# Optimization experiments

Measured on AMD Instinct MI355X. Metric: run time of the kernel, lower is better.

The kernel has to match this reference:

```python
import jax, jax.numpy as jnp
import numpy as np

N = 500_000          # total nodes (25000 graphs x 20 joints)
E = 800_000          # total edges (25000 graphs x 32 edges)
NUM_EDGES = 32       # edges per graph (module init arg)
IN_C = 128
OUT_C = 256
LN_EPS = 1e-5


def setup_inputs() -> dict:
    key = jax.random.key(0)
    ks = jax.random.split(key, 8)
    x = jax.random.normal(ks[0], (N, IN_C), dtype=jnp.float32)
    edge_index = jax.random.randint(ks[1], (2, E), 0, N, dtype=jnp.int64)
    # learned per-graph edge weights (init ones in torch; randomized positive here)
    edge_weights = jax.random.uniform(ks[2], (NUM_EDGES,), jnp.float32, 0.5, 1.5)
    W_gcn = jax.random.normal(ks[3], (IN_C, OUT_C), jnp.float32) / np.float32(np.sqrt(IN_C))
    b_gcn = jnp.zeros((OUT_C,), jnp.float32)
    W_res = jax.random.normal(ks[4], (IN_C, OUT_C), jnp.float32) / np.float32(np.sqrt(IN_C))
    b_res = jnp.zeros((OUT_C,), jnp.float32)
    gamma = jnp.ones((OUT_C,), jnp.float32)
    beta = jnp.zeros((OUT_C,), jnp.float32)
    return dict(x=x, edge_weights=edge_weights, W_gcn=W_gcn, b_gcn=b_gcn,
                W_res=W_res, b_res=b_res, gamma=gamma, beta=beta,
                edge_index=edge_index)


def reference(x, edge_weights, W_gcn, b_gcn, W_res, b_res, gamma, beta, edge_index):
    n = x.shape[0]
    e_tot = edge_index.shape[1]
    batch_size = e_tot // NUM_EDGES
    ew = jnp.tile(edge_weights, batch_size)            # repeated per-batch weights [E]
    row, col = edge_index[0], edge_index[1]            # source -> target

    # GCN symmetric normalization with implicit self loops (weight 1)
    deg = jax.ops.segment_sum(ew, col, num_segments=n) + 1.0   # [N]
    dinv = jax.lax.rsqrt(deg)                                   # [N]
    norm = dinv[row] * ew * dinv[col]                           # [E]

    xw = x @ W_gcn                                              # [N, OUT_C]
    agg = jax.ops.segment_sum(norm[:, None] * xw[row], col, num_segments=n)
    # self-loop contribution: norm_ii = dinv_i * 1 * dinv_i = 1/deg_i
    gcn_out = agg + xw * (dinv * dinv)[:, None] + b_gcn         # [N, OUT_C]

    res = x @ W_res + b_res                                     # residual Linear
    h = gcn_out + res

    mu = jnp.mean(h, axis=-1, keepdims=True)
    var = jnp.mean((h - mu) ** 2, axis=-1, keepdims=True)
    hn = (h - mu) * jax.lax.rsqrt(var + LN_EPS)
    return jax.nn.relu(hn * gamma + beta)
```

## Files before the change

kernel.cpp:

```cpp
#include <hip/hip_runtime.h>
#include <hip/hip_bf16.h>

typedef __attribute__((ext_vector_type(8))) short short8;
typedef __attribute__((ext_vector_type(4))) float f32x4;
typedef unsigned short u16;

#define IN_C 128
#define OUT_C 256
#define LN_EPS 1e-5f
#define CHUNK 320

__device__ __forceinline__ u16 f2bf(float f) {
    __hip_bfloat16 h = __float2bfloat16(f);
    return __builtin_bit_cast(u16, h);
}

__global__ void k_count(const int* __restrict__ ei, const float* __restrict__ ew,
                        float* __restrict__ deg, int* __restrict__ cnt, int E) {
    int e = blockIdx.x * 256 + threadIdx.x;
    if (e < E) {
        int c = ei[E + e];
        atomicAdd(&deg[c], ew[e & 31]);
        atomicAdd(&cnt[c], 1);
    }
}

__global__ void k_dinv(float* __restrict__ deg, int n) {
    int i = blockIdx.x * 256 + threadIdx.x;
    if (i < n) deg[i] = rsqrtf(1.0f + deg[i]);
}

__global__ void k_scan1(const int* __restrict__ cnt, int* __restrict__ partial, int n) {
    __shared__ int sm[256];
    int b = blockIdx.x, t = threadIdx.x;
    int base = b * 1024 + t * 4;
    int s = 0;
#pragma unroll
    for (int k = 0; k < 4; ++k) { int i = base + k; if (i < n) s += cnt[i]; }
    sm[t] = s; __syncthreads();
    for (int m = 128; m > 0; m >>= 1) { if (t < m) sm[t] += sm[t + m]; __syncthreads(); }
    if (t == 0) partial[b] = sm[0];
}

__global__ void k_scan2(int* __restrict__ partial, int nb) {
    __shared__ int sm[512];
    int t = threadIdx.x;
    sm[t] = (t < nb) ? partial[t] : 0;
    __syncthreads();
    for (int d = 1; d < 512; d <<= 1) {
        int v = (t >= d) ? sm[t - d] : 0;
        __syncthreads();
        sm[t] += v;
        __syncthreads();
    }
    if (t < nb) partial[t] = (t == 0) ? 0 : sm[t - 1];
}

__global__ void k_scan3(const int* __restrict__ cnt, const int* __restrict__ partial,
                        int* __restrict__ off, int* __restrict__ cur, int n, int E) {
    __shared__ int sm[256];
    int b = blockIdx.x, t = threadIdx.x;
    int base = b * 1024 + t * 4;
    int c[4]; int s = 0;
#pragma unroll
    for (int k = 0; k < 4; ++k) { int i = base + k; c[k] = (i < n) ? cnt[i] : 0; s += c[k]; }
    sm[t] = s; __syncthreads();
    for (int d = 1; d < 256; d <<= 1) {
        int v = (t >= d) ? sm[t - d] : 0;
        __syncthreads();
        sm[t] += v;
        __syncthreads();
    }
    int run = partial[b] + (sm[t] - s);
#pragma unroll
    for (int k = 0; k < 4; ++k) {
        int i = base + k;
        if (i < n) { off[i] = run; cur[i] = run; }
        run += c[k];
    }
    if (b == 0 && t == 0) off[n] = E;
}

__global__ void k_place(const int* __restrict__ ei, const float* __restrict__ ew,
                        const float* __restrict__ dinv, int* __restrict__ cur,
                        int4* __restrict__ rec4, int E) {
    int e = blockIdx.x * 256 + threadIdx.x;
    if (e >= E) return;
    int r = ei[e], c = ei[E + e];
    float nrm = dinv[r] * ew[e & 31] * dinv[c];
    int p = atomicAdd(&cur[c], 1);
    rec4[p] = make_int4(r, c, __float_as_int(nrm), 0);
}

__global__ void k_wprep(const float* __restrict__ Wg, const float* __restrict__ Wr,
                        const float* __restrict__ bg, const float* __restrict__ br,
                        u16* __restrict__ wfrag, float* __restrict__ bc) {
    int tid = blockIdx.x * 256 + threadIdx.x;
    if (tid < OUT_C) bc[tid] = bg[tid] + br[tid];
    if (tid >= 8192) return;
    int l = tid & 63;
    int t = (tid >> 6) & 15;
    int s = tid >> 10;
    int n = t * 16 + (l & 15);
    int k0 = s * 32 + (l >> 4) * 8;
    short8 pk;
#pragma unroll
    for (int j = 0; j < 8; ++j) {
        int k = k0 + j;
        float w = (k < IN_C) ? Wg[k * OUT_C + n] : Wr[(k - IN_C) * OUT_C + n];
        pk[j] = (short)f2bf(w);
    }
    reinterpret_cast<short8*>(wfrag)[tid] = pk;
}

__global__ __launch_bounds__(512, 4) void k_gemm(
    const float4* __restrict__ x4, const float* __restrict__ dinv,
    const int* __restrict__ off, const int4* __restrict__ rec4,
    const u16* __restrict__ wfrag, const float* __restrict__ bc,
    const float* __restrict__ gamma, const float* __restrict__ beta,
    float* __restrict__ out, int N) {

    __shared__ u16 A[32 * 264];
    __shared__ float red[8 * 32 * 2];
    __shared__ float fin[32 * 2];
    __shared__ int4 recs[CHUNK];

    const int tid = threadIdx.x;
    const int lane = tid & 63;
    const int wv = tid >> 6;
    const long r0 = (long)blockIdx.x * 32;

    const int trow = tid >> 4;
    const int tq = tid & 15;
    const long gr = r0 + trow;

    float ua[8];
    int p0 = 0, p1 = 0;
    {
        u16* xp = &A[trow * 264 + 128 + tq * 8];
        if (gr < N) {
            float d = dinv[gr];
            float d2 = d * d;
            const float4* xs = x4 + gr * 32 + tq * 2;
            float4 v0 = xs[0], v1 = xs[1];
            ushort4 x0, x1;
            x0.x = f2bf(v0.x); x0.y = f2bf(v0.y); x0.z = f2bf(v0.z); x0.w = f2bf(v0.w);
            x1.x = f2bf(v1.x); x1.y = f2bf(v1.y); x1.z = f2bf(v1.z); x1.w = f2bf(v1.w);
            *reinterpret_cast<ushort4*>(xp) = x0;
            *reinterpret_cast<ushort4*>(xp + 4) = x1;
            ua[0] = v0.x * d2; ua[1] = v0.y * d2; ua[2] = v0.z * d2; ua[3] = v0.w * d2;
            ua[4] = v1.x * d2; ua[5] = v1.y * d2; ua[6] = v1.z * d2; ua[7] = v1.w * d2;
            p0 = off[gr]; p1 = off[gr + 1];
        } else {
#pragma unroll
            for (int k = 0; k < 8; ++k) ua[k] = 0.f;
            ushort4 zz = {0, 0, 0, 0};
            *reinterpret_cast<ushort4*>(xp) = zz;
            *reinterpret_cast<ushort4*>(xp + 4) = zz;
        }
    }

    const int rend = (int)((r0 + 32 < N) ? (r0 + 32) : N);
    const int e0 = off[r0];
    const int e1 = off[rend];
    for (int cb = e0; cb < e1; cb += CHUNK) {
        const int ce = (cb + CHUNK < e1) ? (cb + CHUNK) : e1;
        __syncthreads();
        for (int i = tid; i < ce - cb; i += 512) recs[i] = rec4[cb + i];
        __syncthreads();
        const int q0 = (p0 > cb) ? p0 : cb;
        const int q1 = (p1 < ce) ? p1 : ce;
        for (int p = q0; p < q1; p += 4) {
            const int nb = q1 - p;
            int sr[4]; float nr[4];
            float4 ga[4][2];
#pragma unroll
            for (int b = 0; b < 4; ++b) {
                if (b < nb) {
                    int4 rc = recs[p - cb + b];
                    sr[b] = rc.x;
                    nr[b] = __int_as_float(rc.z);
                }
            }
#pragma unroll
            for (int b = 0; b < 4; ++b) {
                if (b < nb) {
                    const float4* xr = x4 + (long)sr[b] * 32 + tq * 2;
                    ga[b][0] = xr[0];
                    ga[b][1] = xr[1];
                }
            }
#pragma unroll
            for (int b = 0; b < 4; ++b) {
                if (b < nb) {
                    ua[0] += nr[b] * ga[b][0].x; ua[1] += nr[b] * ga[b][0].y;
                    ua[2] += nr[b] * ga[b][0].z; ua[3] += nr[b] * ga[b][0].w;
                    ua[4] += nr[b] * ga[b][1].x; ua[5] += nr[b] * ga[b][1].y;
                    ua[6] += nr[b] * ga[b][1].z; ua[7] += nr[b] * ga[b][1].w;
                }
            }
        }
    }

    {
        ushort4 u0, u1;
        u0.x = f2bf(ua[0]); u0.y = f2bf(ua[1]); u0.z = f2bf(ua[2]); u0.w = f2bf(ua[3]);
        u1.x = f2bf(ua[4]); u1.y = f2bf(ua[5]); u1.z = f2bf(ua[6]); u1.w = f2bf(ua[7]);
        u16* up = &A[trow * 264 + tq * 8];
        *reinterpret_cast<ushort4*>(up) = u0;
        *reinterpret_cast<ushort4*>(up + 4) = u1;
    }
    __syncthreads();

    const short8* wf = reinterpret_cast<const short8*>(wfrag);
    short8 bfr[8][2];
#pragma unroll
    for (int s = 0; s < 8; ++s) {
#pragma unroll
        for (int t = 0; t < 2; ++t)
            bfr[s][t] = wf[(s * 16 + (wv * 2 + t)) * 64 + lane];
    }

    f32x4 acc[2][2];
#pragma unroll
    for (int m = 0; m < 2; ++m)
#pragma unroll
        for (int t = 0; t < 2; ++t) acc[m][t] = (f32x4){0.f, 0.f, 0.f, 0.f};

    const int arowb = lane & 15;
    const int koff = (lane >> 4) * 8;
#pragma unroll
    for (int s = 0; s < 8; ++s) {
#pragma unroll
        for (int m = 0; m < 2; ++m) {
            short8 af = *reinterpret_cast<const short8*>(
                &A[(m * 16 + arowb) * 264 + s * 32 + koff]);
#pragma unroll
            for (int t = 0; t < 2; ++t)
                acc[m][t] = __builtin_amdgcn_mfma_f32_16x16x32_bf16(af, bfr[s][t], acc[m][t], 0, 0, 0);
        }
    }

    const int ncol = lane & 15;
    const int g = lane >> 4;
    const float bc0 = bc[wv * 32 + ncol];
    const float bc1 = bc[wv * 32 + 16 + ncol];
#pragma unroll
    for (int m = 0; m < 2; ++m) {
#pragma unroll
        for (int j = 0; j < 4; ++j) {
            float v0 = acc[m][0][j] + bc0;
            float v1 = acc[m][1][j] + bc1;
            acc[m][0][j] = v0;
            acc[m][1][j] = v1;
            float s = v0 + v1;
            float q = v0 * v0 + v1 * v1;
#pragma unroll
            for (int msk = 1; msk < 16; msk <<= 1) {
                s += __shfl_xor(s, msk);
                q += __shfl_xor(q, msk);
            }
            if (ncol == 0) {
                int row = m * 16 + g * 4 + j;
                red[(wv * 32 + row) * 2 + 0] = s;
                red[(wv * 32 + row) * 2 + 1] = q;
            }
        }
    }
    __syncthreads();
    if (tid < 64) {
        int row = tid >> 1, q = tid & 1;
        float t = 0.f;
#pragma unroll
        for (int w = 0; w < 8; ++w) t += red[(w * 32 + row) * 2 + q];
        fin[row * 2 + q] = t;
    }
    __syncthreads();

    const float gv0 = gamma[wv * 32 + ncol], bv0 = beta[wv * 32 + ncol];
    const float gv1 = gamma[wv * 32 + 16 + ncol], bv1 = beta[wv * 32 + 16 + ncol];
#pragma unroll
    for (int m = 0; m < 2; ++m) {
#pragma unroll
        for (int j = 0; j < 4; ++j) {
            int row = m * 16 + g * 4 + j;
            long rr = r0 + row;
            if (rr < N) {
                float mean = fin[row * 2] * (1.f / 256.f);
                float var = fin[row * 2 + 1] * (1.f / 256.f) - mean * mean;
                float rstd = rsqrtf(var + LN_EPS);
                float o0 = (acc[m][0][j] - mean) * rstd * gv0 + bv0;
                float o1 = (acc[m][1][j] - mean) * rstd * gv1 + bv1;
                float* op = out + rr * (long)OUT_C + wv * 32 + ncol;
                op[0]  = fmaxf(o0, 0.f);
                op[16] = fmaxf(o1, 0.f);
            }
        }
    }
}

extern "C" void kernel_launch(void* const* d_in, const int* in_sizes, int n_in,
                              void* d_out, int out_size, void* d_ws, size_t ws_size,
                              hipStream_t stream) {
    const float* x    = (const float*)d_in[0];
    const float* ew   = (const float*)d_in[1];
    const float* Wg   = (const float*)d_in[2];
    const float* bg   = (const float*)d_in[3];
    const float* Wr   = (const float*)d_in[4];
    const float* br   = (const float*)d_in[5];
    const float* gm   = (const float*)d_in[6];
    const float* bt   = (const float*)d_in[7];
    const int*   ei   = (const int*)d_in[8];

    const int N = in_sizes[0] / IN_C;
    const int E = in_sizes[8] / 2;
    const int NB1 = (N + 1023) / 1024;

    int4*  rec4 = (int4*)d_ws;
    float* deg  = (float*)(rec4 + E);
    int*   cnt  = (int*)(deg + N);
    int*   off  = cnt + N;
    int*   cur  = off + N + 1;
    int*   part = cur + N;
    u16*   wfrag = (u16*)(part + 512);
    float* bc   = (float*)(wfrag + 65536);

    hipMemsetAsync(deg, 0, (size_t)N * sizeof(float), stream);
    hipMemsetAsync(cnt, 0, (size_t)N * sizeof(int), stream);
    k_wprep<<<32, 256, 0, stream>>>(Wg, Wr, bg, br, wfrag, bc);
    k_count<<<(E + 255) / 256, 256, 0, stream>>>(ei, ew, deg, cnt, E);
    k_dinv<<<(N + 255) / 256, 256, 0, stream>>>(deg, N);
    k_scan1<<<NB1, 256, 0, stream>>>(cnt, part, N);
    k_scan2<<<1, 512, 0, stream>>>(part, NB1);
    k_scan3<<<NB1, 256, 0, stream>>>(cnt, part, off, cur, N, E);
    k_place<<<(E + 255) / 256, 256, 0, stream>>>(ei, ew, deg, cur, rec4, E);
    k_gemm<<<(N + 31) / 32, 512, 0, stream>>>((const float4*)x, deg, off, rec4,
                                              wfrag, bc, gm, bt, (float*)d_out, N);
}
```

Before: 451.0 us.

## Process 64 rows per GEMM block, hoist weight loads, fold dinv into scan

The fused aggregate+GEMM+LayerNorm kernel now handles 64 rows per block instead of 32. Each thread accumulates two rows, so the register-resident weight fragments are loaded once (now at kernel start) and reused across twice as many MFMA tiles. The standalone rsqrt degree kernel is merged into the first scan pass to drop one launch and one pass over N. The edge-record chunk grows to 512, shared memory doubles, and launch bounds fall to 2 blocks per CU, which lowers occupancy available to hide the random gather latency.

New measurement: 644.1 us. 42.8% more time.

```diff
diff --git a/kernel.cpp b/kernel.cpp
--- a/kernel.cpp
+++ b/kernel.cpp
@@ -8,7 +8,7 @@
 #define IN_C 128
 #define OUT_C 256
 #define LN_EPS 1e-5f
-#define CHUNK 320
+#define CHUNK 512
 
 __device__ __forceinline__ u16 f2bf(float f) {
     __hip_bfloat16 h = __float2bfloat16(f);
@@ -25,18 +25,17 @@
     }
 }
 
-__global__ void k_dinv(float* __restrict__ deg, int n) {
-    int i = blockIdx.x * 256 + threadIdx.x;
-    if (i < n) deg[i] = rsqrtf(1.0f + deg[i]);
-}
-
-__global__ void k_scan1(const int* __restrict__ cnt, int* __restrict__ partial, int n) {
+__global__ void k_scan1(const int* __restrict__ cnt, int* __restrict__ partial,
+                        float* __restrict__ deg, int n) {
     __shared__ int sm[256];
     int b = blockIdx.x, t = threadIdx.x;
     int base = b * 1024 + t * 4;
     int s = 0;
 #pragma unroll
-    for (int k = 0; k < 4; ++k) { int i = base + k; if (i < n) s += cnt[i]; }
+    for (int k = 0; k < 4; ++k) {
+        int i = base + k;
+        if (i < n) { s += cnt[i]; deg[i] = rsqrtf(1.0f + deg[i]); }
+    }
     sm[t] = s; __syncthreads();
     for (int m = 128; m > 0; m >>= 1) { if (t < m) sm[t] += sm[t + m]; __syncthreads(); }
     if (t == 0) partial[b] = sm[0];
@@ -113,54 +112,88 @@
     reinterpret_cast<short8*>(wfrag)[tid] = pk;
 }
 
-__global__ __launch_bounds__(512, 4) void k_gemm(
+__global__ __launch_bounds__(512, 2) void k_gemm(
     const float4* __restrict__ x4, const float* __restrict__ dinv,
     const int* __restrict__ off, const int4* __restrict__ rec4,
     const u16* __restrict__ wfrag, const float* __restrict__ bc,
     const float* __restrict__ gamma, const float* __restrict__ beta,
     float* __restrict__ out, int N) {
 
-    __shared__ u16 A[32 * 264];
-    __shared__ float red[8 * 32 * 2];
-    __shared__ float fin[32 * 2];
+    __shared__ u16 A[64 * 264];
+    __shared__ float red[8 * 64 * 2];
+    __shared__ float fin[64 * 2];
     __shared__ int4 recs[CHUNK];
 
     const int tid = threadIdx.x;
     const int lane = tid & 63;
     const int wv = tid >> 6;
-    const long r0 = (long)blockIdx.x * 32;
+    const long r0 = (long)blockIdx.x * 64;
 
     const int trow = tid >> 4;
     const int tq = tid & 15;
-    const long gr = r0 + trow;
-
-    float ua[8];
-    int p0 = 0, p1 = 0;
+
+    const short8* wf = reinterpret_cast<const short8*>(wfrag);
+    short8 bfr[8][2];
+#pragma unroll
+    for (int s = 0; s < 8; ++s) {
+#pragma unroll
+        for (int t = 0; t < 2; ++t)
+            bfr[s][t] = wf[(s * 16 + (wv * 2 + t)) * 64 + lane];
+    }
+    __builtin_amdgcn_sched_barrier(0);
+
+    float uaA[8], uaB[8];
+    int pA0 = 0, pA1 = 0, pB0 = 0, pB1 = 0;
     {
+        const long grA = r0 + trow;
         u16* xp = &A[trow * 264 + 128 + tq * 8];
-        if (gr < N) {
-            float d = dinv[gr];
+        if (grA < N) {
+            float d = dinv[grA];
             float d2 = d * d;
-            const float4* xs = x4 + gr * 32 + tq * 2;
+            const float4* xs = x4 + grA * 32 + tq * 2;
             float4 v0 = xs[0], v1 = xs[1];
             ushort4 x0, x1;
             x0.x = f2bf(v0.x); x0.y = f2bf(v0.y); x0.z = f2bf(v0.z); x0.w = f2bf(v0.w);
             x1.x = f2bf(v1.x); x1.y = f2bf(v1.y); x1.z = f2bf(v1.z); x1.w = f2bf(v1.w);
             *reinterpret_cast<ushort4*>(xp) = x0;
             *reinterpret_cast<ushort4*>(xp + 4) = x1;
-            ua[0] = v0.x * d2; ua[1] = v0.y * d2; ua[2] = v0.z * d2; ua[3] = v0.w * d2;
-            ua[4] = v1.x * d2; ua[5] = v1.y * d2; ua[6] = v1.z * d2; ua[7] = v1.w * d2;
-            p0 = off[gr]; p1 = off[gr + 1];
+            uaA[0] = v0.x * d2; uaA[1] = v0.y * d2; uaA[2] = v0.z * d2; uaA[3] = v0.w * d2;
+            uaA[4] = v1.x * d2; uaA[5] = v1.y * d2; uaA[6] = v1.z * d2; uaA[7] = v1.w * d2;
+            pA0 = off[grA]; pA1 = off[grA + 1];
         } else {
 #pragma unroll
-            for (int k = 0; k < 8; ++k) ua[k] = 0.f;
+            for (int k = 0; k < 8; ++k) uaA[k] = 0.f;
             ushort4 zz = {0, 0, 0, 0};
             *reinterpret_cast<ushort4*>(xp) = zz;
             *reinterpret_cast<ushort4*>(xp + 4) = zz;
         }
     }
-
-    const int rend = (int)((r0 + 32 < N) ? (r0 + 32) : N);
+    {
+        const long grB = r0 + trow + 32;
+        u16* xp = &A[(trow + 32) * 264 + 128 + tq * 8];
+        if (grB < N) {
+            float d = dinv[grB];
+            float d2 = d * d;
+            const float4* xs = x4 + grB * 32 + tq * 2;
+            float4 v0 = xs[0], v1 = xs[1];
+            ushort4 x0, x1;
+            x0.x = f2bf(v0.x); x0.y = f2bf(v0.y); x0.z = f2bf(v0.z); x0.w = f2bf(v0.w);
+            x1.x = f2bf(v1.x); x1.y = f2bf(v1.y); x1.z = f2bf(v1.z); x1.w = f2bf(v1.w);
+            *reinterpret_cast<ushort4*>(xp) = x0;
+            *reinterpret_cast<ushort4*>(xp + 4) = x1;
+            uaB[0] = v0.x * d2; uaB[1] = v0.y * d2; uaB[2] = v0.z * d2; uaB[3] = v0.w * d2;
+            uaB[4] = v1.x * d2; uaB[5] = v1.y * d2; uaB[6] = v1.z * d2; uaB[7] = v1.w * d2;
+            pB0 = off[grB]; pB1 = off[grB + 1];
+        } else {
+#pragma unroll
+            for (int k = 0; k < 8; ++k) uaB[k] = 0.f;
+            ushort4 zz = {0, 0, 0, 0};
+            *reinterpret_cast<ushort4*>(xp) = zz;
+            *reinterpret_cast<ushort4*>(xp + 4) = zz;
+        }
+    }
+
+    const int rend = (int)((r0 + 64 < N) ? (r0 + 64) : N);
     const int e0 = off[r0];
     const int e1 = off[rend];
     for (int cb = e0; cb < e1; cb += CHUNK) {
@@ -168,62 +201,64 @@
         __syncthreads();
         for (int i = tid; i < ce - cb; i += 512) recs[i] = rec4[cb + i];
         __syncthreads();
-        const int q0 = (p0 > cb) ? p0 : cb;
-        const int q1 = (p1 < ce) ? p1 : ce;
-        for (int p = q0; p < q1; p += 4) {
-            const int nb = q1 - p;
-            int sr[4]; float nr[4];
-            float4 ga[4][2];
-#pragma unroll
-            for (int b = 0; b < 4; ++b) {
-                if (b < nb) {
-                    int4 rc = recs[p - cb + b];
-                    sr[b] = rc.x;
-                    nr[b] = __int_as_float(rc.z);
+#pragma unroll
+        for (int half = 0; half < 2; ++half) {
+            const int rp0 = half ? pB0 : pA0;
+            const int rp1 = half ? pB1 : pA1;
+            float* ua = half ? uaB : uaA;
+            const int q0 = (rp0 > cb) ? rp0 : cb;
+            const int q1 = (rp1 < ce) ? rp1 : ce;
+            for (int p = q0; p < q1; p += 4) {
+                const int nb = q1 - p;
+                int sr[4]; float nr[4];
+                float4 ga[4][2];
+#pragma unroll
+                for (int b = 0; b < 4; ++b) {
+                    if (b < nb) {
+                        int4 rc = recs[p - cb + b];
+                        sr[b] = rc.x;
+                        nr[b] = __int_as_float(rc.z);
+                    }
+                }
+#pragma unroll
+                for (int b = 0; b < 4; ++b) {
+                    if (b < nb) {
+                        const float4* xr = x4 + (long)sr[b] * 32 + tq * 2;
+                        ga[b][0] = xr[0];
+                        ga[b][1] = xr[1];
+                    }
+                }
+#pragma unroll
+                for (int b = 0; b < 4; ++b) {
+                    if (b < nb) {
+                        ua[0] += nr[b] * ga[b][0].x; ua[1] += nr[b] * ga[b][0].y;
+                        ua[2] += nr[b] * ga[b][0].z; ua[3] += nr[b] * ga[b][0].w;
+                        ua[4] += nr[b] * ga[b][1].x; ua[5] += nr[b] * ga[b][1].y;
+                        ua[6] += nr[b] * ga[b][1].z; ua[7] += nr[b] * ga[b][1].w;
+                    }
                 }
             }
-#pragma unroll
-            for (int b = 0; b < 4; ++b) {
-                if (b < nb) {
-                    const float4* xr = x4 + (long)sr[b] * 32 + tq * 2;
-                    ga[b][0] = xr[0];
-                    ga[b][1] = xr[1];
-                }
-            }
-#pragma unroll
-            for (int b = 0; b < 4; ++b) {
-                if (b < nb) {
-                    ua[0] += nr[b] * ga[b][0].x; ua[1] += nr[b] * ga[b][0].y;
-                    ua[2] += nr[b] * ga[b][0].z; ua[3] += nr[b] * ga[b][0].w;
-                    ua[4] += nr[b] * ga[b][1].x; ua[5] += nr[b] * ga[b][1].y;
-                    ua[6] += nr[b] * ga[b][1].z; ua[7] += nr[b] * ga[b][1].w;
-                }
-            }
         }
     }
 
     {
         ushort4 u0, u1;
-        u0.x = f2bf(ua[0]); u0.y = f2bf(ua[1]); u0.z = f2bf(ua[2]); u0.w = f2bf(ua[3]);
-        u1.x = f2bf(ua[4]); u1.y = f2bf(ua[5]); u1.z = f2bf(ua[6]); u1.w = f2bf(ua[7]);
+        u0.x = f2bf(uaA[0]); u0.y = f2bf(uaA[1]); u0.z = f2bf(uaA[2]); u0.w = f2bf(uaA[3]);
+        u1.x = f2bf(uaA[4]); u1.y = f2bf(uaA[5]); u1.z = f2bf(uaA[6]); u1.w = f2bf(uaA[7]);
         u16* up = &A[trow * 264 + tq * 8];
         *reinterpret_cast<ushort4*>(up) = u0;
         *reinterpret_cast<ushort4*>(up + 4) = u1;
+        u0.x = f2bf(uaB[0]); u0.y = f2bf(uaB[1]); u0.z = f2bf(uaB[2]); u0.w = f2bf(uaB[3]);
+        u1.x = f2bf(uaB[4]); u1.y = f2bf(uaB[5]); u1.z = f2bf(uaB[6]); u1.w = f2bf(uaB[7]);
+        up = &A[(trow + 32) * 264 + tq * 8];
+        *reinterpret_cast<ushort4*>(up) = u0;
+        *reinterpret_cast<ushort4*>(up + 4) = u1;
     }
     __syncthreads();
 
-    const short8* wf = reinterpret_cast<const short8*>(wfrag);
-    short8 bfr[8][2];
-#pragma unroll
-    for (int s = 0; s < 8; ++s) {
-#pragma unroll
-        for (int t = 0; t < 2; ++t)
-            bfr[s][t] = wf[(s * 16 + (wv * 2 + t)) * 64 + lane];
-    }
-
-    f32x4 acc[2][2];
-#pragma unroll
-    for (int m = 0; m < 2; ++m)
+    f32x4 acc[4][2];
+#pragma unroll
+    for (int m = 0; m < 4; ++m)
 #pragma unroll
         for (int t = 0; t < 2; ++t) acc[m][t] = (f32x4){0.f, 0.f, 0.f, 0.f};
 
@@ -232,7 +267,7 @@
 #pragma unroll
     for (int s = 0; s < 8; ++s) {
 #pragma unroll
-        for (int m = 0; m < 2; ++m) {
+        for (int m = 0; m < 4; ++m) {
             short8 af = *reinterpret_cast<const short8*>(
                 &A[(m * 16 + arowb) * 264 + s * 32 + koff]);
 #pragma unroll
@@ -246,7 +281,7 @@
     const float bc0 = bc[wv * 32 + ncol];
     const float bc1 = bc[wv * 32 + 16 + ncol];
 #pragma unroll
-    for (int m = 0; m < 2; ++m) {
+    for (int m = 0; m < 4; ++m) {
 #pragma unroll
         for (int j = 0; j < 4; ++j) {
             float v0 = acc[m][0][j] + bc0;
@@ -262,17 +297,17 @@
             }
             if (ncol == 0) {
                 int row = m * 16 + g * 4 + j;
-                red[(wv * 32 + row) * 2 + 0] = s;
-                red[(wv * 32 + row) * 2 + 1] = q;
+                red[(wv * 64 + row) * 2 + 0] = s;
+                red[(wv * 64 + row) * 2 + 1] = q;
             }
         }
     }
     __syncthreads();
-    if (tid < 64) {
+    if (tid < 128) {
         int row = tid >> 1, q = tid & 1;
         float t = 0.f;
 #pragma unroll
-        for (int w = 0; w < 8; ++w) t += red[(w * 32 + row) * 2 + q];
+        for (int w = 0; w < 8; ++w) t += red[(w * 64 + row) * 2 + q];
         fin[row * 2 + q] = t;
     }
     __syncthreads();
@@ -280,7 +315,7 @@
     const float gv0 = gamma[wv * 32 + ncol], bv0 = beta[wv * 32 + ncol];
     const float gv1 = gamma[wv * 32 + 16 + ncol], bv1 = beta[wv * 32 + 16 + ncol];
 #pragma unroll
-    for (int m = 0; m < 2; ++m) {
+    for (int m = 0; m < 4; ++m) {
 #pragma unroll
         for (int j = 0; j < 4; ++j) {
             int row = m * 16 + g * 4 + j;
@@ -329,11 +364,10 @@
     hipMemsetAsync(cnt, 0, (size_t)N * sizeof(int), stream);
     k_wprep<<<32, 256, 0, stream>>>(Wg, Wr, bg, br, wfrag, bc);
     k_count<<<(E + 255) / 256, 256, 0, stream>>>(ei, ew, deg, cnt, E);
-    k_dinv<<<(N + 255) / 256, 256, 0, stream>>>(deg, N);
-    k_scan1<<<NB1, 256, 0, stream>>>(cnt, part, N);
+    k_scan1<<<NB1, 256, 0, stream>>>(cnt, part, deg, N);
     k_scan2<<<1, 512, 0, stream>>>(part, NB1);
     k_scan3<<<NB1, 256, 0, stream>>>(cnt, part, off, cur, N, E);
     k_place<<<(E + 255) / 256, 256, 0, stream>>>(ei, ew, deg, cur, rec4, E);
-    k_gemm<<<(N + 31) / 32, 512, 0, stream>>>((const float4*)x, deg, off, rec4,
+    k_gemm<<<(N + 63) / 64, 512, 0, stream>>>((const float4*)x, deg, off, rec4,
                                               wfrag, bc, gm, bt, (float*)d_out, N);
 }
```
